# Kernel tuning notes

Measured on AMD Instinct MI355X. Metric: run time of the kernel, lower is better.

The kernel has to match this reference:

```python
import jax, jax.numpy as jnp
import numpy as np

B, DIM, NH, HD, H, W = 4, 64, 8, 8, 256, 256  # head_dim must equal num_heads (scale broadcast)


def setup_inputs() -> dict:
    key = jax.random.key(0)
    ks = jax.random.split(key, 10)
    s = 0.05
    return {
        "x": jax.random.normal(ks[0], (B, DIM, H, W), jnp.float32),
        "w3": jax.random.normal(ks[1], (DIM, 1, 3, 3), jnp.float32) * s,  # depthwise 3x3
        "b3": jax.random.normal(ks[2], (DIM,), jnp.float32) * s,
        "w5": jax.random.normal(ks[3], (DIM, 1, 5, 5), jnp.float32) * s,  # depthwise 5x5
        "b5": jax.random.normal(ks[4], (DIM,), jnp.float32) * s,
        "wqkv": jax.random.normal(ks[5], (3 * DIM, DIM), jnp.float32) * s,  # 1x1 conv, no bias
        "scale": jnp.ones((NH, 1, 1), jnp.float32),
        "g1_w": jax.random.normal(ks[6], (DIM // 4, DIM), jnp.float32) * s,
        "g1_b": jnp.zeros((DIM // 4,), jnp.float32),
        "g2_w": jax.random.normal(ks[7], (2, DIM // 4), jnp.float32) * s,
        "g2_b": jnp.zeros((2,), jnp.float32),
        "wp": jax.random.normal(ks[8], (DIM, DIM), jnp.float32) * s,  # 1x1 proj
        "bp": jnp.zeros((DIM,), jnp.float32),
    }


def _dwconv(x, w, b, pad):
    out = jax.lax.conv_general_dilated(
        x, w, (1, 1), [(pad, pad), (pad, pad)],
        dimension_numbers=("NCHW", "OIHW", "NCHW"), feature_group_count=x.shape[1])
    return out + b[None, :, None, None]


def _l2norm(t, eps=1e-12):  # F.normalize(dim=-1)
    n = jnp.sqrt(jnp.sum(t * t, axis=-1, keepdims=True))
    return t / jnp.maximum(n, eps)


def reference(x, w3, b3, w5, b5, wqkv, scale, g1_w, g1_b, g2_w, g2_b, wp, bp):
    b, c, h, w = x.shape
    conv_feat = _dwconv(x, w3, b3, 1) + _dwconv(x, w5, b5, 2)

    qkv = jnp.einsum("oc,bchw->bohw", wqkv, x)          # [b,3c,h,w]
    qkv = qkv.reshape(b, 3, NH, HD, h * w)
    q, k, v = qkv[:, 0], qkv[:, 1], qkv[:, 2]           # [b,NH,HD,hw]
    q = _l2norm(q)
    k = _l2norm(k)

    q_h = q.reshape(b, NH, HD, h, w)
    k_h = k.reshape(b, NH, HD, h, w)
    v_h = v.reshape(b, NH, HD, h, w)

    # row-axis attention: per (b,head,d-channel) attention over rows x (scale broadcasts onto HD axis)
    attn_h = jnp.einsum("bhdxy,bhdzy->bhdxz", q_h, k_h) * scale   # [b,NH,HD,h,h]
    attn_h = jax.nn.softmax(attn_h, axis=-1)
    out_h = jnp.einsum("bhdxz,bhdzy->bhdxy", attn_h, v_h).reshape(b, c, h, w)

    # column-axis attention (operate on transposed spatial layout)
    q_v = jnp.swapaxes(q_h, -1, -2)                      # [b,NH,HD,w,h]
    k_v = jnp.swapaxes(k_h, -1, -2)
    v_v = jnp.swapaxes(v_h, -1, -2)
    attn_v = jnp.einsum("bhdyx,bhdzx->bhdyz", q_v, k_v) * scale   # [b,NH,HD,w,w]
    attn_v = jax.nn.softmax(attn_v, axis=-1)
    out_v = jnp.einsum("bhdyz,bhdzx->bhdyx", attn_v, v_v)         # [b,NH,HD,w,h]
    out_v = jnp.swapaxes(out_v, -1, -2).reshape(b, c, h, w)

    attn_feat = out_h + out_v

    # global-pool gating: softmax over 2 mixing weights
    gx = jnp.mean(x, axis=(2, 3))                        # [b,c]
    h1 = jax.nn.relu(gx @ g1_w.T + g1_b)
    gw = jax.nn.softmax(h1 @ g2_w.T + g2_b, axis=1)      # [b,2]
    cw = gw[:, 0][:, None, None, None]
    aw = gw[:, 1][:, None, None, None]

    out = cw * conv_feat + aw * attn_feat
    return jnp.einsum("oc,bchw->bohw", wp, out) + bp[None, :, None, None]
```

## Files before the change

### kernel.cpp

```cpp
#include <hip/hip_runtime.h>
#include <stdint.h>


typedef unsigned short u16;
typedef __attribute__((ext_vector_type(8))) short bf16x8;
typedef __attribute__((ext_vector_type(4))) float f32x4;

#define DEV static __device__ __forceinline__

DEV u16 f2bf(float f) {
  unsigned u = __float_as_uint(f);
  return (u16)((u + 0x7fffu + ((u >> 16) & 1u)) >> 16);
}
DEV float bf2f(u16 h) { return __uint_as_float(((unsigned)h) << 16); }

__global__ void k_gx(const float* __restrict__ x, float* __restrict__ gxsum) {
  int bc = blockIdx.x, t = threadIdx.x;
  const float4* p = (const float4*)(x + ((size_t)bc << 16));
  float s = 0.f;
  for (int i = 0; i < 64; ++i) { float4 v = p[t + 256 * i]; s += v.x + v.y + v.z + v.w; }
  for (int off = 32; off; off >>= 1) s += __shfl_down(s, off);
  __shared__ float lds[4];
  if ((t & 63) == 0) lds[t >> 6] = s;
  __syncthreads();
  if (t == 0) gxsum[bc] = lds[0] + lds[1] + lds[2] + lds[3];
}

__global__ void k_gate(const float* __restrict__ gxsum, const float* __restrict__ g1w,
                       const float* __restrict__ g1b, const float* __restrict__ g2w,
                       const float* __restrict__ g2b, float* __restrict__ cwaw) {
  __shared__ float h1[4][16];
  int t = threadIdx.x;
  int b = t >> 4, j = t & 15;
  float a = g1b[j];
  for (int c = 0; c < 64; ++c) a += g1w[j * 64 + c] * gxsum[b * 64 + c] * (1.f / 65536.f);
  h1[b][j] = fmaxf(a, 0.f);
  __syncthreads();
  if (t < 4) {
    float l0 = g2b[0], l1 = g2b[1];
    for (int k = 0; k < 16; ++k) { l0 += g2w[k] * h1[t][k]; l1 += g2w[16 + k] * h1[t][k]; }
    float m = fmaxf(l0, l1);
    float e0 = __expf(l0 - m), e1 = __expf(l1 - m);
    float inv = 1.f / (e0 + e1);
    cwaw[t * 2 + 0] = e0 * inv;
    cwaw[t * 2 + 1] = e1 * inv;
  }
}

__global__ __launch_bounds__(256) void k_qkv(const float* __restrict__ x,
                                             const float* __restrict__ wqkv,
                                             u16* __restrict__ qkv) {
  __shared__ u16 Ws[192 * 72];
  __shared__ u16 Xs[128 * 72];
  int t = threadIdx.x;
  int b = blockIdx.x >> 9;
  int p0 = (blockIdx.x & 511) << 7;

  {
    int row = t >> 2, c0 = (t & 3) << 4;
#pragma unroll
    for (int i = 0; i < 3; ++i) {
      int r = i * 64 + row;
      const float* src = wqkv + r * 64 + c0;
      unsigned pk[8];
#pragma unroll
      for (int j = 0; j < 8; ++j)
        pk[j] = (unsigned)f2bf(src[2 * j]) | ((unsigned)f2bf(src[2 * j + 1]) << 16);
      uint4* dst = (uint4*)&Ws[r * 72 + c0];
      dst[0] = make_uint4(pk[0], pk[1], pk[2], pk[3]);
      dst[1] = make_uint4(pk[4], pk[5], pk[6], pk[7]);
    }
  }
  {
    int p = t & 127, ch = t >> 7;
    const float* xb = x + ((size_t)(b * 64) << 16) + p0 + p;
#pragma unroll
    for (int i = 0; i < 32; ++i) {
      int c = 2 * i + ch;
      Xs[p * 72 + c] = f2bf(xb[(size_t)c << 16]);
    }
  }
  __syncthreads();

  int w = t >> 6, l = t & 63, q = l >> 4, cl = l & 15;
  bf16x8 af[3][2];
#pragma unroll
  for (int g = 0; g < 3; ++g)
#pragma unroll
    for (int k = 0; k < 2; ++k)
      af[g][k] = *(const bf16x8*)&Ws[(w * 48 + g * 16 + cl) * 72 + k * 32 + q * 8];

  f32x4 acc[3][8];
  f32x4 zero = {0.f, 0.f, 0.f, 0.f};
#pragma unroll
  for (int g = 0; g < 3; ++g)
#pragma unroll
    for (int j = 0; j < 8; ++j) acc[g][j] = zero;

  for (int j = 0; j < 8; ++j) {
    bf16x8 b0 = *(const bf16x8*)&Xs[(j * 16 + cl) * 72 + q * 8];
    bf16x8 b1 = *(const bf16x8*)&Xs[(j * 16 + cl) * 72 + 32 + q * 8];
#pragma unroll
    for (int g = 0; g < 3; ++g) {
      acc[g][j] = __builtin_amdgcn_mfma_f32_16x16x32_bf16(af[g][0], b0, acc[g][j], 0, 0, 0);
      acc[g][j] = __builtin_amdgcn_mfma_f32_16x16x32_bf16(af[g][1], b1, acc[g][j], 0, 0, 0);
    }
  }
  u16* outb = qkv + ((size_t)(b * 192) << 16) + p0;
  for (int g = 0; g < 3; ++g) {
    int rowb = w * 48 + g * 16 + q * 4;
#pragma unroll
    for (int r = 0; r < 4; ++r) {
      u16* orow = outb + ((size_t)(rowb + r) << 16);
#pragma unroll
      for (int j = 0; j < 8; ++j) orow[j * 16 + cl] = f2bf(acc[g][j][r]);
    }
  }
}

__global__ void k_rnorm(const u16* __restrict__ qkv, float* __restrict__ rnorm) {
  int b = blockIdx.x >> 7, ch = blockIdx.x & 127;
  const uint2* p2 = (const uint2*)(qkv + ((size_t)(b * 192 + ch) << 16));
  int t = threadIdx.x;
  float s = 0.f;
  for (int i = 0; i < 64; ++i) {
    uint2 v = p2[t + 256 * i];
    float a = bf2f(v.x & 0xffff), bq = bf2f(v.x >> 16);
    float c = bf2f(v.y & 0xffff), d = bf2f(v.y >> 16);
    s += a * a + bq * bq + c * c + d * d;
  }
  for (int off = 32; off; off >>= 1) s += __shfl_down(s, off);
  __shared__ float lds[4];
  if ((t & 63) == 0) lds[t >> 6] = s;
  __syncthreads();
  if (t == 0) {
    float tot = lds[0] + lds[1] + lds[2] + lds[3];
    rnorm[blockIdx.x] = 1.f / fmaxf(sqrtf(tot), 1e-12f);
  }
}

__global__ void k_conv(const float* __restrict__ x, const float* __restrict__ w3,
                       const float* __restrict__ b3, const float* __restrict__ w5,
                       const float* __restrict__ b5, const float* __restrict__ cwaw,
                       float* __restrict__ outmix) {
  int rt = blockIdx.x & 31, bc = blockIdx.x >> 5, c = bc & 63, b = bc >> 6;
  int r0 = rt * 8;
  const float* xp = x + ((size_t)bc << 16);
  __shared__ float xs[12][256];
  int y = threadIdx.x;
  for (int rr = 0; rr < 12; ++rr) {
    int gr = r0 - 2 + rr;
    xs[rr][y] = (gr >= 0 && gr < 256) ? xp[(size_t)gr * 256 + y] : 0.f;
  }
  __syncthreads();
  float W3[9], W5[25];
#pragma unroll
  for (int i = 0; i < 9; ++i) W3[i] = w3[c * 9 + i];
#pragma unroll
  for (int i = 0; i < 25; ++i) W5[i] = w5[c * 25 + i];
  float bias = b3[c] + b5[c];
  float cw = cwaw[b * 2];
  float* op = outmix + ((size_t)bc << 16);
  for (int k = 0; k < 8; ++k) {
    float a = bias;
#pragma unroll
    for (int di = 0; di < 3; ++di)
#pragma unroll
      for (int dj = 0; dj < 3; ++dj) {
        int yy = y + dj - 1;
        float xv = (yy >= 0 && yy < 256) ? xs[k + 1 + di][yy] : 0.f;
        a += W3[di * 3 + dj] * xv;
      }
#pragma unroll
    for (int di = 0; di < 5; ++di)
#pragma unroll
      for (int dj = 0; dj < 5; ++dj) {
        int yy = y + dj - 2;
        float xv = (yy >= 0 && yy < 256) ? xs[k + di][yy] : 0.f;
        a += W5[di * 5 + dj] * xv;
      }
    op[(size_t)(r0 + k) * 256 + y] = cw * a;
  }
}

__global__ __launch_bounds__(256) void k_attn(
    const u16* __restrict__ qkv, const float* __restrict__ rnorm,
    const float* __restrict__ scale, u16* __restrict__ oh, u16* __restrict__ ov) {
  __shared__ __align__(16) unsigned char smem[54272];
  u16* Pls = (u16*)smem;
  unsigned* Qt32 = (unsigned*)smem;
  float* red = (float*)(smem + 33792);
  unsigned* Tt32 = (unsigned*)(smem + 33792);
  float* Osf = (float*)smem;

  int t = threadIdx.x;
  int w = t >> 6, l = t & 63, q = l >> 4, cl = l & 15;
  int idx = (blockIdx.x & 7) * 256 + (blockIdx.x >> 3);
  int rt = idx & 3, dir = (idx >> 2) & 1, c = (idx >> 3) & 63, b = idx >> 9;
  int r0 = rt << 6;

  const size_t P = 65536;
  const u16* Qp = qkv + (size_t)(b * 192 + c) * P;
  const u16* Kp = qkv + (size_t)(b * 192 + 64 + c) * P;
  const u16* Vp = qkv + (size_t)(b * 192 + 128 + c) * P;

  float sc = rnorm[b * 128 + c] * rnorm[b * 128 + 64 + c] * scale[c >> 3];

  f32x4 Sa[4][4];
  f32x4 zero = {0.f, 0.f, 0.f, 0.f};
#pragma unroll
  for (int i = 0; i < 4; ++i)
#pragma unroll
    for (int j = 0; j < 4; ++j) Sa[i][j] = zero;

  if (dir == 0) {
    for (int yw = 0; yw < 8; ++yw) {
      int y0 = yw << 5;
      bf16x8 af[4], bfr[4];
#pragma unroll
      for (int i = 0; i < 4; ++i)
        af[i] = *(const bf16x8*)&Qp[(size_t)(r0 + i * 16 + cl) * 256 + y0 + q * 8];
#pragma unroll
      for (int j = 0; j < 4; ++j)
        bfr[j] = *(const bf16x8*)&Kp[(size_t)(w * 64 + j * 16 + cl) * 256 + y0 + q * 8];
#pragma unroll
      for (int i = 0; i < 4; ++i)
#pragma unroll
        for (int j = 0; j < 4; ++j)
          Sa[i][j] = __builtin_amdgcn_mfma_f32_16x16x32_bf16(af[i], bfr[j], Sa[i][j], 0, 0, 0);
    }
  } else {
    int y2 = t >> 4, colc = t & 15;
    int kkey = (((y2 >> 2) ^ (colc & 3)) << 2) + (y2 & 3);
    int qkey = (((y2 >> 2) ^ ((colc >> 2) & 3)) << 2) + (y2 & 3);
    for (int yw = 0; yw < 8; ++yw) {
      int y0 = yw << 5;
      const u16* krp = Kp + (size_t)(y0 + 2 * y2) * 256 + colc * 16;
      uint4 ka0 = *(const uint4*)krp;
      uint4 ka1 = *(const uint4*)(krp + 8);
      uint4 kb0 = *(const uint4*)(krp + 256);
      uint4 kb1 = *(const uint4*)(krp + 264);
      const u16* qrp = Qp + (size_t)(y0 + 2 * y2) * 256 + r0 + colc * 4;
      uint2 qa = *(const uint2*)qrp;
      uint2 qb = *(const uint2*)(qrp + 256);
      unsigned KA[8] = {ka0.x, ka0.y, ka0.z, ka0.w, ka1.x, ka1.y, ka1.z, ka1.w};
      unsigned KB[8] = {kb0.x, kb0.y, kb0.z, kb0.w, kb1.x, kb1.y, kb1.z, kb1.w};
      unsigned QA[2] = {qa.x, qa.y};
      unsigned QB[2] = {qb.x, qb.y};
      __syncthreads();
#pragma unroll
      for (int m = 0; m < 16; ++m) {
        unsigned lo = (m & 1) ? (KA[m >> 1] >> 16) : (KA[m >> 1] & 0xffffu);
        unsigned hi = (m & 1) ? (KB[m >> 1] & 0xffff0000u) : (KB[m >> 1] << 16);
        Tt32[(colc * 16 + m) * 20 + kkey] = lo | hi;
      }
#pragma unroll
      for (int m = 0; m < 4; ++m) {
        unsigned lo = (m & 1) ? (QA[m >> 1] >> 16) : (QA[m >> 1] & 0xffffu);
        unsigned hi = (m & 1) ? (QB[m >> 1] & 0xffff0000u) : (QB[m >> 1] << 16);
        Qt32[(colc * 4 + m) * 20 + qkey] = lo | hi;
      }
      __syncthreads();
      bf16x8 af[4], bfr[4];
#pragma unroll
      for (int i = 0; i < 4; ++i)
        af[i] = *(const bf16x8*)&Qt32[(i * 16 + cl) * 20 + ((q ^ i) << 2)];
#pragma unroll
      for (int j = 0; j < 4; ++j) {
        int col = w * 64 + j * 16 + cl;
        bfr[j] = *(const bf16x8*)&Tt32[col * 20 + ((q ^ j) << 2)];
      }
#pragma unroll
      for (int i = 0; i < 4; ++i)
#pragma unroll
        for (int j = 0; j < 4; ++j)
          Sa[i][j] = __builtin_amdgcn_mfma_f32_16x16x32_bf16(af[i], bfr[j], Sa[i][j], 0, 0, 0);
    }
    __syncthreads();
  }

  float sm[4][4];
#pragma unroll
  for (int i = 0; i < 4; ++i)
#pragma unroll
    for (int r = 0; r < 4; ++r) {
      float s0 = 0.f;
#pragma unroll
      for (int j = 0; j < 4; ++j) {
        float e = __expf(Sa[i][j][r] * sc);
        Sa[i][j][r] = e;
        s0 += e;
      }
#pragma unroll
      for (int off = 1; off < 16; off <<= 1) s0 += __shfl_xor(s0, off);
      sm[i][r] = s0;
    }
  if (cl == 0) {
#pragma unroll
    for (int i = 0; i < 4; ++i)
#pragma unroll
      for (int r = 0; r < 4; ++r) red[w * 64 + i * 16 + q * 4 + r] = sm[i][r];
  }
  __syncthreads();
#pragma unroll
  for (int i = 0; i < 4; ++i)
#pragma unroll
    for (int r = 0; r < 4; ++r) {
      int rho = i * 16 + q * 4 + r;
      sm[i][r] = 1.f / (red[rho] + red[64 + rho] + red[128 + rho] + red[192 + rho]);
    }
#pragma unroll
  for (int i = 0; i < 4; ++i)
#pragma unroll
    for (int r = 0; r < 4; ++r) {
      int rho = i * 16 + q * 4 + r;
#pragma unroll
      for (int j = 0; j < 4; ++j)
        Pls[rho * 264 + w * 64 + j * 16 + cl] = f2bf(Sa[i][j][r] * sm[i][r]);
    }
  __syncthreads();

  f32x4 Oa[4][4];
#pragma unroll
  for (int i = 0; i < 4; ++i)
#pragma unroll
    for (int j = 0; j < 4; ++j) Oa[i][j] = zero;

  if (dir == 0) {
    int z2 = t >> 4, colc = t & 15;
    int zlo = z2 & 3;
    int wkey = (((z2 >> 2) ^ (colc & 3)) << 2) + zlo;
    for (int zw = 0; zw < 8; ++zw) {
      int z0 = zw << 5;
      const u16* rp = Vp + (size_t)(z0 + 2 * z2) * 256 + colc * 16;
      uint4 a0 = *(const uint4*)rp;
      uint4 a1 = *(const uint4*)(rp + 8);
      uint4 c0 = *(const uint4*)(rp + 256);
      uint4 c1 = *(const uint4*)(rp + 264);
      unsigned A[8] = {a0.x, a0.y, a0.z, a0.w, a1.x, a1.y, a1.z, a1.w};
      unsigned Bv[8] = {c0.x, c0.y, c0.z, c0.w, c1.x, c1.y, c1.z, c1.w};
      __syncthreads();
#pragma unroll
      for (int m = 0; m < 16; ++m) {
        unsigned lo = (m & 1) ? (A[m >> 1] >> 16) : (A[m >> 1] & 0xffffu);
        unsigned hi = (m & 1) ? (Bv[m >> 1] & 0xffff0000u) : (Bv[m >> 1] << 16);
        Tt32[(colc * 16 + m) * 20 + wkey] = lo | hi;
      }
      __syncthreads();
      bf16x8 af[4], bfr[4];
#pragma unroll
      for (int i = 0; i < 4; ++i)
        af[i] = *(const bf16x8*)&Pls[(i * 16 + cl) * 264 + z0 + q * 8];
#pragma unroll
      for (int j = 0; j < 4; ++j) {
        int col = w * 64 + j * 16 + cl;
        bfr[j] = *(const bf16x8*)&Tt32[col * 20 + ((q ^ j) << 2)];
      }
#pragma unroll
      for (int i = 0; i < 4; ++i)
#pragma unroll
        for (int j = 0; j < 4; ++j)
          Oa[i][j] = __builtin_amdgcn_mfma_f32_16x16x32_bf16(af[i], bfr[j], Oa[i][j], 0, 0, 0);
    }
    u16* op = oh + (size_t)(b * 64 + c) * P;
#pragma unroll
    for (int i = 0; i < 4; ++i)
#pragma unroll
      for (int j = 0; j < 4; ++j)
#pragma unroll
        for (int r = 0; r < 4; ++r)
          op[(size_t)(r0 + i * 16 + q * 4 + r) * 256 + w * 64 + j * 16 + cl] = f2bf(Oa[i][j][r]);
  } else {
    for (int zw = 0; zw < 8; ++zw) {
      int z0 = zw << 5;
      bf16x8 af[4], bfr[4];
#pragma unroll
      for (int i = 0; i < 4; ++i)
        af[i] = *(const bf16x8*)&Pls[(i * 16 + cl) * 264 + z0 + q * 8];
#pragma unroll
      for (int j = 0; j < 4; ++j)
        bfr[j] = *(const bf16x8*)&Vp[(size_t)(w * 64 + j * 16 + cl) * 256 + z0 + q * 8];
#pragma unroll
      for (int i = 0; i < 4; ++i)
#pragma unroll
        for (int j = 0; j < 4; ++j)
          Oa[i][j] = __builtin_amdgcn_mfma_f32_16x16x32_bf16(af[i], bfr[j], Oa[i][j], 0, 0, 0);
    }
    u16* op = ov + (size_t)(b * 64 + c) * P;
    __syncthreads();
    for (int h = 0; h < 2; ++h) {
#pragma unroll
      for (int ii = 0; ii < 2; ++ii) {
        int i = h * 2 + ii;
#pragma unroll
        for (int j = 0; j < 4; ++j)
#pragma unroll
          for (int r = 0; r < 4; ++r)
            Osf[(ii * 16 + q * 4 + r) * 260 + w * 64 + j * 16 + cl] = Oa[i][j][r];
      }
      __syncthreads();
      int rr = t & 31, xb = t >> 5;
      for (int xx = 0; xx < 32; ++xx) {
        int xcol = xx * 8 + xb;
        op[(size_t)xcol * 256 + r0 + h * 32 + rr] = f2bf(Osf[rr * 260 + xcol]);
      }
      __syncthreads();
    }
  }
}

__global__ __launch_bounds__(256) void k_final(
    float* __restrict__ dout, const u16* __restrict__ oh, const u16* __restrict__ ov,
    const float* __restrict__ wp, const float* __restrict__ bp,
    const float* __restrict__ cwaw) {
  __shared__ u16 Ms[256 * 72];
  __shared__ u16 Ws[64 * 72];
  int t = threadIdx.x;
  int b = blockIdx.x >> 8;
  int p0 = (blockIdx.x & 255) << 8;
  float aw = cwaw[b * 2 + 1];

  {
    int row = t >> 2, c0 = (t & 3) << 4;
    const float* src = wp + row * 64 + c0;
    unsigned pk[8];
#pragma unroll
    for (int j = 0; j < 8; ++j)
      pk[j] = (unsigned)f2bf(src[2 * j]) | ((unsigned)f2bf(src[2 * j + 1]) << 16);
    uint4* dst = (uint4*)&Ws[row * 72 + c0];
    dst[0] = make_uint4(pk[0], pk[1], pk[2], pk[3]);
    dst[1] = make_uint4(pk[4], pk[5], pk[6], pk[7]);
  }
  {
    size_t base = ((size_t)(b * 64) << 16) + p0 + t;
    for (int c = 0; c < 64; ++c) {
      size_t off = base + ((size_t)c << 16);
      float m = dout[off] + aw * (bf2f(oh[off]) + bf2f(ov[off]));
      Ms[t * 72 + c] = f2bf(m);
    }
  }
  __syncthreads();

  int w = t >> 6, l = t & 63, q = l >> 4, cl = l & 15;
  bf16x8 af0 = *(const bf16x8*)&Ws[(w * 16 + cl) * 72 + q * 8];
  bf16x8 af1 = *(const bf16x8*)&Ws[(w * 16 + cl) * 72 + 32 + q * 8];

  f32x4 acc[16];
  f32x4 zero = {0.f, 0.f, 0.f, 0.f};
#pragma unroll
  for (int j = 0; j < 16; ++j) acc[j] = zero;

  for (int j = 0; j < 16; ++j) {
    bf16x8 b0 = *(const bf16x8*)&Ms[(j * 16 + cl) * 72 + q * 8];
    bf16x8 b1 = *(const bf16x8*)&Ms[(j * 16 + cl) * 72 + 32 + q * 8];
    acc[j] = __builtin_amdgcn_mfma_f32_16x16x32_bf16(af0, b0, acc[j], 0, 0, 0);
    acc[j] = __builtin_amdgcn_mfma_f32_16x16x32_bf16(af1, b1, acc[j], 0, 0, 0);
  }

  float bpv[4];
#pragma unroll
  for (int r = 0; r < 4; ++r) bpv[r] = bp[w * 16 + q * 4 + r];
  float* outb = dout + ((size_t)(b * 64) << 16) + p0;
#pragma unroll
  for (int r = 0; r < 4; ++r) {
    float* orow = outb + ((size_t)(w * 16 + q * 4 + r) << 16);
#pragma unroll
    for (int j = 0; j < 16; ++j) orow[j * 16 + cl] = acc[j][r] + bpv[r];
  }
}

extern "C" void kernel_launch(void* const* d_in, const int* in_sizes, int n_in,
                              void* d_out, int out_size, void* d_ws, size_t ws_size,
                              hipStream_t stream) {
  const float* x = (const float*)d_in[0];
  const float* w3 = (const float*)d_in[1];
  const float* b3 = (const float*)d_in[2];
  const float* w5 = (const float*)d_in[3];
  const float* b5 = (const float*)d_in[4];
  const float* wqkv = (const float*)d_in[5];
  const float* scale = (const float*)d_in[6];
  const float* g1w = (const float*)d_in[7];
  const float* g1b = (const float*)d_in[8];
  const float* g2w = (const float*)d_in[9];
  const float* g2b = (const float*)d_in[10];
  const float* wp = (const float*)d_in[11];
  const float* bp = (const float*)d_in[12];
  float* out = (float*)d_out;

  char* ws = (char*)d_ws;
  u16* qkv = (u16*)(ws);
  u16* ohb = (u16*)(ws + 100663296ull);
  u16* ovb = (u16*)(ws + 134217728ull);
  float* fs = (float*)(ws + 167772160ull);
  float* gxsum = fs;
  float* cwaw = fs + 256;
  float* rnorm = fs + 264;

  k_gx<<<256, 256, 0, stream>>>(x, gxsum);
  k_gate<<<1, 64, 0, stream>>>(gxsum, g1w, g1b, g2w, g2b, cwaw);
  k_qkv<<<2048, 256, 0, stream>>>(x, wqkv, qkv);
  k_rnorm<<<512, 256, 0, stream>>>(qkv, rnorm);
  k_conv<<<8192, 256, 0, stream>>>(x, w3, b3, w5, b5, cwaw, out);
  k_attn<<<2048, 256, 0, stream>>>(qkv, rnorm, scale, ohb, ovb);
  k_final<<<1024, 256, 0, stream>>>(out, ohb, ovb, wp, bp, cwaw);
}
```

Measured before the change: 355.0 us.

## Prefetch next K/Q/V tile into registers during transposed-path MFMA loops

In the transposed attention paths, the global loads for the next 32-row tile of K/Q (and V) are issued before the second barrier, so their latency overlaps the LDS transpose and the MFMA work of the current tile. The full __syncthreads is replaced by an LDS-only wait plus s_barrier, and s_setprio is raised around the MFMA blocks. The depthwise conv tile gets zero-padded halo columns in shared memory, which removes per-tap bounds checks. Costs are higher register pressure from the double-buffered fragments and a fully unrolled loop.

```diff
diff --git a/kernel.cpp b/kernel.cpp
--- a/kernel.cpp
+++ b/kernel.cpp
@@ -13,6 +13,11 @@
   return (u16)((u + 0x7fffu + ((u >> 16) & 1u)) >> 16);
 }
 DEV float bf2f(u16 h) { return __uint_as_float(((unsigned)h) << 16); }
+
+DEV void bar_lds() {
+  asm volatile("s_waitcnt lgkmcnt(0)" ::: "memory");
+  __builtin_amdgcn_s_barrier();
+}
 
 __global__ void k_gx(const float* __restrict__ x, float* __restrict__ gxsum) {
   int bc = blockIdx.x, t = threadIdx.x;
@@ -146,11 +151,14 @@
   int rt = blockIdx.x & 31, bc = blockIdx.x >> 5, c = bc & 63, b = bc >> 6;
   int r0 = rt * 8;
   const float* xp = x + ((size_t)bc << 16);
-  __shared__ float xs[12][256];
+  __shared__ float xs[12][260];
   int y = threadIdx.x;
   for (int rr = 0; rr < 12; ++rr) {
     int gr = r0 - 2 + rr;
-    xs[rr][y] = (gr >= 0 && gr < 256) ? xp[(size_t)gr * 256 + y] : 0.f;
+    xs[rr][y + 2] = (gr >= 0 && gr < 256) ? xp[(size_t)gr * 256 + y] : 0.f;
+  }
+  if (y < 2) {
+    for (int rr = 0; rr < 12; ++rr) { xs[rr][y] = 0.f; xs[rr][258 + y] = 0.f; }
   }
   __syncthreads();
   float W3[9], W5[25];
@@ -166,19 +174,13 @@
 #pragma unroll
     for (int di = 0; di < 3; ++di)
 #pragma unroll
-      for (int dj = 0; dj < 3; ++dj) {
-        int yy = y + dj - 1;
-        float xv = (yy >= 0 && yy < 256) ? xs[k + 1 + di][yy] : 0.f;
-        a += W3[di * 3 + dj] * xv;
-      }
+      for (int dj = 0; dj < 3; ++dj)
+        a += W3[di * 3 + dj] * xs[k + 1 + di][y + 1 + dj];
 #pragma unroll
     for (int di = 0; di < 5; ++di)
 #pragma unroll
-      for (int dj = 0; dj < 5; ++dj) {
-        int yy = y + dj - 2;
-        float xv = (yy >= 0 && yy < 256) ? xs[k + di][yy] : 0.f;
-        a += W5[di * 5 + dj] * xv;
-      }
+      for (int dj = 0; dj < 5; ++dj)
+        a += W5[di * 5 + dj] * xs[k + di][y + dj];
     op[(size_t)(r0 + k) * 256 + y] = cw * a;
   }
 }
@@ -223,31 +225,37 @@
 #pragma unroll
       for (int j = 0; j < 4; ++j)
         bfr[j] = *(const bf16x8*)&Kp[(size_t)(w * 64 + j * 16 + cl) * 256 + y0 + q * 8];
+      __builtin_amdgcn_s_setprio(1);
 #pragma unroll
       for (int i = 0; i < 4; ++i)
 #pragma unroll
         for (int j = 0; j < 4; ++j)
           Sa[i][j] = __builtin_amdgcn_mfma_f32_16x16x32_bf16(af[i], bfr[j], Sa[i][j], 0, 0, 0);
+      __builtin_amdgcn_s_setprio(0);
     }
   } else {
     int y2 = t >> 4, colc = t & 15;
     int kkey = (((y2 >> 2) ^ (colc & 3)) << 2) + (y2 & 3);
     int qkey = (((y2 >> 2) ^ ((colc >> 2) & 3)) << 2) + (y2 & 3);
-    for (int yw = 0; yw < 8; ++yw) {
-      int y0 = yw << 5;
-      const u16* krp = Kp + (size_t)(y0 + 2 * y2) * 256 + colc * 16;
+    unsigned KA[8], KB[8], QA[2], QB[2];
+    {
+      const u16* krp = Kp + (size_t)(2 * y2) * 256 + colc * 16;
       uint4 ka0 = *(const uint4*)krp;
       uint4 ka1 = *(const uint4*)(krp + 8);
       uint4 kb0 = *(const uint4*)(krp + 256);
       uint4 kb1 = *(const uint4*)(krp + 264);
-      const u16* qrp = Qp + (size_t)(y0 + 2 * y2) * 256 + r0 + colc * 4;
+      const u16* qrp = Qp + (size_t)(2 * y2) * 256 + r0 + colc * 4;
       uint2 qa = *(const uint2*)qrp;
       uint2 qb = *(const uint2*)(qrp + 256);
-      unsigned KA[8] = {ka0.x, ka0.y, ka0.z, ka0.w, ka1.x, ka1.y, ka1.z, ka1.w};
-      unsigned KB[8] = {kb0.x, kb0.y, kb0.z, kb0.w, kb1.x, kb1.y, kb1.z, kb1.w};
-      unsigned QA[2] = {qa.x, qa.y};
-      unsigned QB[2] = {qb.x, qb.y};
-      __syncthreads();
+      KA[0] = ka0.x; KA[1] = ka0.y; KA[2] = ka0.z; KA[3] = ka0.w;
+      KA[4] = ka1.x; KA[5] = ka1.y; KA[6] = ka1.z; KA[7] = ka1.w;
+      KB[0] = kb0.x; KB[1] = kb0.y; KB[2] = kb0.z; KB[3] = kb0.w;
+      KB[4] = kb1.x; KB[5] = kb1.y; KB[6] = kb1.z; KB[7] = kb1.w;
+      QA[0] = qa.x; QA[1] = qa.y; QB[0] = qb.x; QB[1] = qb.y;
+    }
+#pragma unroll
+    for (int yw = 0; yw < 8; ++yw) {
+      bar_lds();
 #pragma unroll
       for (int m = 0; m < 16; ++m) {
         unsigned lo = (m & 1) ? (KA[m >> 1] >> 16) : (KA[m >> 1] & 0xffffu);
@@ -260,7 +268,24 @@
         unsigned hi = (m & 1) ? (QB[m >> 1] & 0xffff0000u) : (QB[m >> 1] << 16);
         Qt32[(colc * 4 + m) * 20 + qkey] = lo | hi;
       }
-      __syncthreads();
+      unsigned NKA[8], NKB[8], NQA[2], NQB[2];
+      if (yw < 7) {
+        int y0 = (yw + 1) << 5;
+        const u16* krp = Kp + (size_t)(y0 + 2 * y2) * 256 + colc * 16;
+        uint4 ka0 = *(const uint4*)krp;
+        uint4 ka1 = *(const uint4*)(krp + 8);
+        uint4 kb0 = *(const uint4*)(krp + 256);
+        uint4 kb1 = *(const uint4*)(krp + 264);
+        const u16* qrp = Qp + (size_t)(y0 + 2 * y2) * 256 + r0 + colc * 4;
+        uint2 qa = *(const uint2*)qrp;
+        uint2 qb = *(const uint2*)(qrp + 256);
+        NKA[0] = ka0.x; NKA[1] = ka0.y; NKA[2] = ka0.z; NKA[3] = ka0.w;
+        NKA[4] = ka1.x; NKA[5] = ka1.y; NKA[6] = ka1.z; NKA[7] = ka1.w;
+        NKB[0] = kb0.x; NKB[1] = kb0.y; NKB[2] = kb0.z; NKB[3] = kb0.w;
+        NKB[4] = kb1.x; NKB[5] = kb1.y; NKB[6] = kb1.z; NKB[7] = kb1.w;
+        NQA[0] = qa.x; NQA[1] = qa.y; NQB[0] = qb.x; NQB[1] = qb.y;
+      }
+      bar_lds();
       bf16x8 af[4], bfr[4];
 #pragma unroll
       for (int i = 0; i < 4; ++i)
@@ -270,11 +295,18 @@
         int col = w * 64 + j * 16 + cl;
         bfr[j] = *(const bf16x8*)&Tt32[col * 20 + ((q ^ j) << 2)];
       }
+      __builtin_amdgcn_s_setprio(1);
 #pragma unroll
       for (int i = 0; i < 4; ++i)
 #pragma unroll
         for (int j = 0; j < 4; ++j)
           Sa[i][j] = __builtin_amdgcn_mfma_f32_16x16x32_bf16(af[i], bfr[j], Sa[i][j], 0, 0, 0);
+      __builtin_amdgcn_s_setprio(0);
+      if (yw < 7) {
+#pragma unroll
+        for (int m = 0; m < 8; ++m) { KA[m] = NKA[m]; KB[m] = NKB[m]; }
+        QA[0] = NQA[0]; QA[1] = NQA[1]; QB[0] = NQB[0]; QB[1] = NQB[1];
+      }
     }
     __syncthreads();
   }
@@ -330,23 +362,41 @@
     int z2 = t >> 4, colc = t & 15;
     int zlo = z2 & 3;
     int wkey = (((z2 >> 2) ^ (colc & 3)) << 2) + zlo;
-    for (int zw = 0; zw < 8; ++zw) {
-      int z0 = zw << 5;
-      const u16* rp = Vp + (size_t)(z0 + 2 * z2) * 256 + colc * 16;
+    unsigned A[8], Bv[8];
+    {
+      const u16* rp = Vp + (size_t)(2 * z2) * 256 + colc * 16;
       uint4 a0 = *(const uint4*)rp;
       uint4 a1 = *(const uint4*)(rp + 8);
       uint4 c0 = *(const uint4*)(rp + 256);
       uint4 c1 = *(const uint4*)(rp + 264);
-      unsigned A[8] = {a0.x, a0.y, a0.z, a0.w, a1.x, a1.y, a1.z, a1.w};
-      unsigned Bv[8] = {c0.x, c0.y, c0.z, c0.w, c1.x, c1.y, c1.z, c1.w};
-      __syncthreads();
+      A[0] = a0.x; A[1] = a0.y; A[2] = a0.z; A[3] = a0.w;
+      A[4] = a1.x; A[5] = a1.y; A[6] = a1.z; A[7] = a1.w;
+      Bv[0] = c0.x; Bv[1] = c0.y; Bv[2] = c0.z; Bv[3] = c0.w;
+      Bv[4] = c1.x; Bv[5] = c1.y; Bv[6] = c1.z; Bv[7] = c1.w;
+    }
+#pragma unroll
+    for (int zw = 0; zw < 8; ++zw) {
+      int z0 = zw << 5;
+      bar_lds();
 #pragma unroll
       for (int m = 0; m < 16; ++m) {
         unsigned lo = (m & 1) ? (A[m >> 1] >> 16) : (A[m >> 1] & 0xffffu);
         unsigned hi = (m & 1) ? (Bv[m >> 1] & 0xffff0000u) : (Bv[m >> 1] << 16);
         Tt32[(colc * 16 + m) * 20 + wkey] = lo | hi;
       }
-      __syncthreads();
+      unsigned NA[8], NBv[8];
+      if (zw < 7) {
+        const u16* rp = Vp + (size_t)(z0 + 32 + 2 * z2) * 256 + colc * 16;
+        uint4 a0 = *(const uint4*)rp;
+        uint4 a1 = *(const uint4*)(rp + 8);
+        uint4 c0 = *(const uint4*)(rp + 256);
+        uint4 c1 = *(const uint4*)(rp + 264);
+        NA[0] = a0.x; NA[1] = a0.y; NA[2] = a0.z; NA[3] = a0.w;
+        NA[4] = a1.x; NA[5] = a1.y; NA[6] = a1.z; NA[7] = a1.w;
+        NBv[0] = c0.x; NBv[1] = c0.y; NBv[2] = c0.z; NBv[3] = c0.w;
+        NBv[4] = c1.x; NBv[5] = c1.y; NBv[6] = c1.z; NBv[7] = c1.w;
+      }
+      bar_lds();
       bf16x8 af[4], bfr[4];
 #pragma unroll
       for (int i = 0; i < 4; ++i)
@@ -356,11 +406,17 @@
         int col = w * 64 + j * 16 + cl;
         bfr[j] = *(const bf16x8*)&Tt32[col * 20 + ((q ^ j) << 2)];
       }
+      __builtin_amdgcn_s_setprio(1);
 #pragma unroll
       for (int i = 0; i < 4; ++i)
 #pragma unroll
         for (int j = 0; j < 4; ++j)
           Oa[i][j] = __builtin_amdgcn_mfma_f32_16x16x32_bf16(af[i], bfr[j], Oa[i][j], 0, 0, 0);
+      __builtin_amdgcn_s_setprio(0);
+      if (zw < 7) {
+#pragma unroll
+        for (int m = 0; m < 8; ++m) { A[m] = NA[m]; Bv[m] = NBv[m]; }
+      }
     }
     u16* op = oh + (size_t)(b * 64 + c) * P;
 #pragma unroll
@@ -380,11 +436,13 @@
 #pragma unroll
       for (int j = 0; j < 4; ++j)
         bfr[j] = *(const bf16x8*)&Vp[(size_t)(w * 64 + j * 16 + cl) * 256 + z0 + q * 8];
+      __builtin_amdgcn_s_setprio(1);
 #pragma unroll
       for (int i = 0; i < 4; ++i)
 #pragma unroll
         for (int j = 0; j < 4; ++j)
           Oa[i][j] = __builtin_amdgcn_mfma_f32_16x16x32_bf16(af[i], bfr[j], Oa[i][j], 0, 0, 0);
+      __builtin_amdgcn_s_setprio(0);
     }
     u16* op = ov + (size_t)(b * 64 + c) * P;
     __syncthreads();
```

Result: faster. 338.4 us (-4.7%).
